# Kernel optimization log

Measured on AMD Instinct MI355X. Metric: run time of the kernel, lower is better.

Reference implementation:

```python
import jax, jax.numpy as jnp
import numpy as np

N_NODES = 100000
N_EDGES = 3200000
D_FEAT = 32


def setup_inputs() -> dict:
    key = jax.random.key(0)
    k1, k2, k3 = jax.random.split(key, 3)
    inp = jax.random.normal(k1, (N_NODES, D_FEAT), dtype=jnp.float32)
    eidx = jax.random.randint(k2, (2, N_EDGES), 0, N_NODES, dtype=jnp.int64)
    enorm = jax.random.uniform(k3, (N_EDGES,), dtype=jnp.float32)
    esgn = jnp.ones((N_EDGES,), dtype=jnp.float32)
    return {"input": inp, "eidx": eidx, "enorm": enorm, "esgn": esgn}


def reference(input, eidx, enorm, esgn):
    # Gather source node features, scale by sign * norm, scatter-add to targets.
    sidx, tidx = eidx[0], eidx[1]
    message = input[sidx] * (esgn * enorm)[:, None]  # [n_edges, d]
    res = jax.ops.segment_sum(message, tidx, num_segments=input.shape[0])
    return res.astype(input.dtype)
```

## Files before the change

### kernel.cpp

```cpp
#include <hip/hip_runtime.h>


#define G    256
#define KMAX 1024
#define SPAN_SHIFT 7
#define SPAN 128
#define CAP  6144
#define NB   256

__global__ __launch_bounds__(1024) void hist_kernel(
    const int* __restrict__ tidx, int* __restrict__ cnt,
    int n_edges, int epb, int vec)
{
    __shared__ int lh[KMAX];
    int g = blockIdx.x, t = threadIdx.x;
    lh[t] = 0;
    __syncthreads();
    int beg = g * epb;
    int lim = beg + epb; if (lim > n_edges) lim = n_edges;
    if (vec) {
        int nq = (lim > beg) ? ((lim - beg) >> 2) : 0;
        for (int q = t; q < nq; q += 1024) {
            int4 tn = *(const int4*)(tidx + beg + q * 4);
            atomicAdd(&lh[tn.x >> SPAN_SHIFT], 1);
            atomicAdd(&lh[tn.y >> SPAN_SHIFT], 1);
            atomicAdd(&lh[tn.z >> SPAN_SHIFT], 1);
            atomicAdd(&lh[tn.w >> SPAN_SHIFT], 1);
        }
        for (int e = beg + (nq << 2) + t; e < lim; e += 1024)
            atomicAdd(&lh[tidx[e] >> SPAN_SHIFT], 1);
    } else {
        for (int e = beg + t; e < lim; e += 1024)
            atomicAdd(&lh[tidx[e] >> SPAN_SHIFT], 1);
    }
    __syncthreads();
    cnt[g * KMAX + t] = lh[t];
}

__global__ __launch_bounds__(1024) void scatter_kernel(
    const int* __restrict__ sidx, const int* __restrict__ tidx,
    const float* __restrict__ enorm, const float* __restrict__ esgn,
    const int* __restrict__ cnt, int* __restrict__ tot,
    int2* __restrict__ recs, int n_edges, int epb, int vec)
{
    __shared__ int gbase[KMAX];
    __shared__ int lh[KMAX];
    __shared__ int part[KMAX];
    int g = blockIdx.x, t = threadIdx.x;

    int run = 0, my = 0;
    for (int gp = 0; gp < G; ++gp) {
        if (gp == g) my = run;
        run += cnt[gp * KMAX + t];
    }
    if (g == 0) tot[t] = run;
    part[t] = run;
    __syncthreads();
    for (int off = 1; off < KMAX; off <<= 1) {
        int v = (t >= off) ? part[t - off] : 0;
        __syncthreads();
        part[t] += v;
        __syncthreads();
    }
    gbase[t] = (part[t] - run) + my;
    lh[t] = 0;
    __syncthreads();

    int beg = g * epb;
    int lim = beg + epb; if (lim > n_edges) lim = n_edges;

    #define SCAT_EDGE(tn_, sn_, w_) {                                        \
        int b_ = (tn_) >> SPAN_SHIFT;                                        \
        int rank_ = atomicAdd(&lh[b_], 1);                                   \
        unsigned rec_ = ((unsigned)(sn_) << SPAN_SHIFT) |                    \
                        (unsigned)((tn_) & (SPAN - 1));                      \
        recs[gbase[b_] + rank_] = make_int2((int)rec_, __float_as_int(w_)); }

    if (vec) {
        int nq = (lim > beg) ? ((lim - beg) >> 2) : 0;
        for (int q = t; q < nq; q += 1024) {
            int e = beg + q * 4;
            int4   tn = *(const int4*)(tidx + e);
            int4   sn = *(const int4*)(sidx + e);
            float4 nw = *(const float4*)(enorm + e);
            float4 sw = *(const float4*)(esgn + e);
            SCAT_EDGE(tn.x, sn.x, nw.x * sw.x);
            SCAT_EDGE(tn.y, sn.y, nw.y * sw.y);
            SCAT_EDGE(tn.z, sn.z, nw.z * sw.z);
            SCAT_EDGE(tn.w, sn.w, nw.w * sw.w);
        }
        for (int e = beg + (nq << 2) + t; e < lim; e += 1024) {
            int tn = tidx[e]; int sn = sidx[e];
            float w = enorm[e] * esgn[e];
            SCAT_EDGE(tn, sn, w);
        }
    } else {
        for (int e = beg + t; e < lim; e += 1024) {
            int tn = tidx[e]; int sn = sidx[e];
            float w = enorm[e] * esgn[e];
            SCAT_EDGE(tn, sn, w);
        }
    }
    #undef SCAT_EDGE
}

__global__ __launch_bounds__(1024) void bucket_accum(
    const float* __restrict__ input, const int2* __restrict__ recs,
    const int* __restrict__ tot, float* __restrict__ out, int n_nodes)
{
    __shared__ int2 srec[CAP];
    __shared__ int part[KMAX];
    __shared__ int lcnt[SPAN];
    __shared__ int lbeg[SPAN];
    __shared__ int lcur[SPAN];
    __shared__ int sb[2];
    int b = blockIdx.x;
    int t = threadIdx.x;

    int c = tot[t];
    part[t] = c;
    __syncthreads();
    for (int off = 1; off < KMAX; off <<= 1) {
        int v = (t >= off) ? part[t - off] : 0;
        __syncthreads();
        part[t] += v;
        __syncthreads();
    }
    if (t == b) { sb[0] = part[t] - c; sb[1] = part[t]; }
    __syncthreads();
    int bstart = sb[0], bend = sb[1];
    int base_node = b << SPAN_SHIFT;

    if (bend - bstart <= CAP) {
        if (t < SPAN) lcnt[t] = 0;
        __syncthreads();
        for (int i = bstart + t; i < bend; i += 1024)
            atomicAdd(&lcnt[recs[i].x & (SPAN - 1)], 1);
        __syncthreads();
        int cc = (t < SPAN) ? lcnt[t] : 0;
        if (t < SPAN) lbeg[t] = cc;
        __syncthreads();
        for (int off = 1; off < SPAN; off <<= 1) {
            int v = (t < SPAN && t >= off) ? lbeg[t - off] : 0;
            __syncthreads();
            if (t < SPAN) lbeg[t] += v;
            __syncthreads();
        }
        if (t < SPAN) {
            int excl = lbeg[t] - cc;
            lbeg[t] = excl;
            lcur[t] = excl;
        }
        __syncthreads();
        for (int i = bstart + t; i < bend; i += 1024) {
            int2 r = recs[i];
            int pos = atomicAdd(&lcur[r.x & (SPAN - 1)], 1);
            srec[pos] = r;
        }
        __syncthreads();
        int node = t >> 3;
        int lane = t & 7;
        int beg = lbeg[node];
        int end = beg + lcnt[node];
        float4 acc = make_float4(0.f, 0.f, 0.f, 0.f);
        int i = beg;

        #define GAT1(qq)                                                     \
            float4 v##qq = ((const float4*)(input +                          \
                (size_t)(((unsigned)q##qq.x) >> SPAN_SHIFT) * 32))[lane];    \
            float w##qq = __int_as_float(q##qq.y);
        #define FMA1(qq)                                                     \
            acc.x = fmaf(w##qq, v##qq.x, acc.x);                             \
            acc.y = fmaf(w##qq, v##qq.y, acc.y);                             \
            acc.z = fmaf(w##qq, v##qq.z, acc.z);                             \
            acc.w = fmaf(w##qq, v##qq.w, acc.w);

        for (; i + 7 < end; i += 8) {
            int2 q0 = srec[i];     int2 q1 = srec[i + 1];
            int2 q2 = srec[i + 2]; int2 q3 = srec[i + 3];
            int2 q4 = srec[i + 4]; int2 q5 = srec[i + 5];
            int2 q6 = srec[i + 6]; int2 q7 = srec[i + 7];
            GAT1(0) GAT1(1) GAT1(2) GAT1(3)
            GAT1(4) GAT1(5) GAT1(6) GAT1(7)
            FMA1(0) FMA1(1) FMA1(2) FMA1(3)
            FMA1(4) FMA1(5) FMA1(6) FMA1(7)
        }
        for (; i + 3 < end; i += 4) {
            int2 q0 = srec[i];     int2 q1 = srec[i + 1];
            int2 q2 = srec[i + 2]; int2 q3 = srec[i + 3];
            GAT1(0) GAT1(1) GAT1(2) GAT1(3)
            FMA1(0) FMA1(1) FMA1(2) FMA1(3)
        }
        for (; i < end; ++i) {
            int2 q0 = srec[i];
            GAT1(0)
            FMA1(0)
        }
        #undef GAT1
        #undef FMA1

        int gnode = base_node + node;
        if (gnode < n_nodes)
            ((float4*)(out + (size_t)gnode * 32))[lane] = acc;
    } else {
        for (int i = t; i < SPAN * 32; i += 1024) {
            int gn = base_node + (i >> 5);
            if (gn < n_nodes) out[(size_t)gn * 32 + (i & 31)] = 0.f;
        }
        __syncthreads();
        for (int i = bstart + t; i < bend; i += 1024) {
            int2 r = recs[i];
            float w = __int_as_float(r.y);
            int s = (int)(((unsigned)r.x) >> SPAN_SHIFT);
            int gn = base_node + (r.x & (SPAN - 1));
            if (gn < n_nodes)
                for (int j = 0; j < 32; ++j)
                    atomicAdd(&out[(size_t)gn * 32 + j], w * input[(size_t)s * 32 + j]);
        }
    }
}

__global__ __launch_bounds__(NB) void graphconv_scatter(
    const float* __restrict__ input, const int* __restrict__ sidx,
    const int* __restrict__ tidx, const float* __restrict__ enorm,
    const float* __restrict__ esgn, float* __restrict__ out, int n_edges)
{
    int t = blockIdx.x * NB + threadIdx.x;
    int e = t >> 3;
    int sub = t & 7;
    if (e >= n_edges) return;
    int s = sidx[e];
    int d = tidx[e];
    float w = enorm[e] * esgn[e];
    const float4* src = (const float4*)(input + (size_t)s * 32);
    float4 v = src[sub];
    float* op = out + (size_t)d * 32 + sub * 4;
    atomicAdd(op + 0, v.x * w);
    atomicAdd(op + 1, v.y * w);
    atomicAdd(op + 2, v.z * w);
    atomicAdd(op + 3, v.w * w);
}

extern "C" void kernel_launch(void* const* d_in, const int* in_sizes, int n_in,
                              void* d_out, int out_size, void* d_ws, size_t ws_size,
                              hipStream_t stream) {
    const float* input = (const float*)d_in[0];
    const int*   eidx  = (const int*)d_in[1];
    const float* enorm = (const float*)d_in[2];
    const float* esgn  = (const float*)d_in[3];
    float*       out   = (float*)d_out;

    int n_edges = in_sizes[1] / 2;
    int n_nodes = in_sizes[0] / 32;
    const int* sidx = eidx;
    const int* tidx = eidx + n_edges;

    int K = (n_nodes + SPAN - 1) >> SPAN_SHIFT;

    size_t need = (size_t)n_edges * 8 +
                  ((size_t)G * KMAX + KMAX) * 4;

    if (ws_size >= need && K <= KMAX) {
        int2* recs  = (int2*)d_ws;
        int*  cnt   = (int*)(recs + n_edges);
        int*  tot   = cnt + (size_t)G * KMAX;

        int epb = ((n_edges + G - 1) / G + 3) & ~3;
        int vec = ((n_edges & 3) == 0 &&
                   (((uintptr_t)tidx | (uintptr_t)sidx |
                     (uintptr_t)enorm | (uintptr_t)esgn) & 15) == 0) ? 1 : 0;

        hist_kernel   <<<G,    1024, 0, stream>>>(tidx, cnt, n_edges, epb, vec);
        scatter_kernel<<<G,    1024, 0, stream>>>(sidx, tidx, enorm, esgn,
                                                  cnt, tot, recs,
                                                  n_edges, epb, vec);
        bucket_accum  <<<K,    1024, 0, stream>>>(input, recs, tot,
                                                  out, n_nodes);
    } else {
        hipMemsetAsync(d_out, 0, (size_t)out_size * sizeof(float), stream);
        size_t threads_total = (size_t)n_edges * 8;
        int grid = (int)((threads_total + NB - 1) / NB);
        graphconv_scatter<<<grid, NB, 0, stream>>>(input, sidx, tidx, enorm, esgn,
                                                   out, n_edges);
    }
}
```

Baseline: 208.7 us.

## Move per-bucket cross-block prefix scan into a separate parallel scan kernel

Previously every scatter block serially read all G block-count rows (256 loads per thread) to compute its exclusive offset and the totals, so the same 1 MB of counts was re-read by every block. A new scan1_kernel with one block per bucket computes the cross-block exclusive prefix and totals once. The scatter kernel then loads only its own prefix row plus the totals. This adds a kernel launch and an extra 1 MB workspace array.

```diff
diff --git a/kernel.cpp b/kernel.cpp
--- a/kernel.cpp
+++ b/kernel.cpp
@@ -37,10 +37,28 @@
     cnt[g * KMAX + t] = lh[t];
 }
 
+__global__ __launch_bounds__(G) void scan1_kernel(
+    const int* __restrict__ cnt, int* __restrict__ pref, int* __restrict__ tot)
+{
+    __shared__ int part[G];
+    int b = blockIdx.x, t = threadIdx.x;
+    int c = cnt[t * KMAX + b];
+    part[t] = c;
+    __syncthreads();
+    for (int off = 1; off < G; off <<= 1) {
+        int v = (t >= off) ? part[t - off] : 0;
+        __syncthreads();
+        part[t] += v;
+        __syncthreads();
+    }
+    pref[t * KMAX + b] = part[t] - c;
+    if (t == G - 1) tot[b] = part[t];
+}
+
 __global__ __launch_bounds__(1024) void scatter_kernel(
     const int* __restrict__ sidx, const int* __restrict__ tidx,
     const float* __restrict__ enorm, const float* __restrict__ esgn,
-    const int* __restrict__ cnt, int* __restrict__ tot,
+    const int* __restrict__ tot, const int* __restrict__ pref,
     int2* __restrict__ recs, int n_edges, int epb, int vec)
 {
     __shared__ int gbase[KMAX];
@@ -48,13 +66,8 @@
     __shared__ int part[KMAX];
     int g = blockIdx.x, t = threadIdx.x;
 
-    int run = 0, my = 0;
-    for (int gp = 0; gp < G; ++gp) {
-        if (gp == g) my = run;
-        run += cnt[gp * KMAX + t];
-    }
-    if (g == 0) tot[t] = run;
-    part[t] = run;
+    int c = tot[t];
+    part[t] = c;
     __syncthreads();
     for (int off = 1; off < KMAX; off <<= 1) {
         int v = (t >= off) ? part[t - off] : 0;
@@ -62,7 +75,7 @@
         part[t] += v;
         __syncthreads();
     }
-    gbase[t] = (part[t] - run) + my;
+    gbase[t] = (part[t] - c) + pref[g * KMAX + t];
     lh[t] = 0;
     __syncthreads();
 
@@ -258,12 +271,13 @@
     int K = (n_nodes + SPAN - 1) >> SPAN_SHIFT;
 
     size_t need = (size_t)n_edges * 8 +
-                  ((size_t)G * KMAX + KMAX) * 4;
+                  ((size_t)2 * G * KMAX + KMAX) * 4;
 
     if (ws_size >= need && K <= KMAX) {
         int2* recs  = (int2*)d_ws;
         int*  cnt   = (int*)(recs + n_edges);
-        int*  tot   = cnt + (size_t)G * KMAX;
+        int*  pref  = cnt + (size_t)G * KMAX;
+        int*  tot   = pref + (size_t)G * KMAX;
 
         int epb = ((n_edges + G - 1) / G + 3) & ~3;
         int vec = ((n_edges & 3) == 0 &&
@@ -271,8 +285,9 @@
                      (uintptr_t)enorm | (uintptr_t)esgn) & 15) == 0) ? 1 : 0;
 
         hist_kernel   <<<G,    1024, 0, stream>>>(tidx, cnt, n_edges, epb, vec);
+        scan1_kernel  <<<KMAX, G,    0, stream>>>(cnt, pref, tot);
         scatter_kernel<<<G,    1024, 0, stream>>>(sidx, tidx, enorm, esgn,
-                                                  cnt, tot, recs,
+                                                  tot, pref, recs,
                                                   n_edges, epb, vec);
         bucket_accum  <<<K,    1024, 0, stream>>>(input, recs, tot,
                                                   out, n_nodes);
```

Result: faster. 199.2 us (-4.5%).
